# Kernel optimization log

Hardware: AMD Instinct MI355X
Metric: run time of the kernel (lower is better)

## Reference

```python
import jax, jax.numpy as jnp
import numpy as np

N = 4096      # total instances in the bag
S = 64        # number of images (segments), idx_list has S+1 boundaries
L = 500
D = 128
FLAT = 50 * 4 * 4  # 800


def _conv(x, w, b):
    # x: [N,C,H,W], w: [O,I,5,5], VALID conv, stride 1
    y = jax.lax.conv_general_dilated(x, w, (1, 1), 'VALID',
                                     dimension_numbers=('NCHW', 'OIHW', 'NCHW'))
    return y + b[None, :, None, None]


def _maxpool2(x):
    return jax.lax.reduce_window(x, -jnp.inf, jax.lax.max,
                                 (1, 1, 2, 2), (1, 1, 2, 2), 'VALID')


def setup_inputs() -> dict:
    key = jax.random.key(0)
    ks = jax.random.split(key, 18)
    def p(k, shape, fan):
        return jax.random.normal(k, shape, jnp.float32) * np.float32(1.0 / np.sqrt(fan))
    x = jax.random.normal(ks[0], (1, N, 3, 28, 28), jnp.float32)
    idx_list = (jnp.arange(S + 1, dtype=jnp.int32) * (N // S))  # sorted boundaries 0..N
    return {
        'x': x,
        'idx_list': idx_list,
        'conv1_w': p(ks[1], (20, 3, 5, 5), 3 * 25), 'conv1_b': jnp.zeros((20,), jnp.float32),
        'conv2_w': p(ks[2], (50, 20, 5, 5), 20 * 25), 'conv2_b': jnp.zeros((50,), jnp.float32),
        'fc_w': p(ks[3], (FLAT, L), FLAT), 'fc_b': jnp.zeros((L,), jnp.float32),
        'a1_w1': p(ks[4], (L, D), L), 'a1_b1': jnp.zeros((D,), jnp.float32),
        'a1_w2': p(ks[5], (D, 1), D), 'a1_b2': jnp.zeros((1,), jnp.float32),
        'a2_w1': p(ks[6], (L, D), L), 'a2_b1': jnp.zeros((D,), jnp.float32),
        'a2_w2': p(ks[7], (D, 1), D), 'a2_b2': jnp.zeros((1,), jnp.float32),
        'clf_w': p(ks[8], (L, 1), L), 'clf_b': jnp.zeros((1,), jnp.float32),
    }


def reference(x, idx_list, conv1_w, conv1_b, conv2_w, conv2_b, fc_w, fc_b,
              a1_w1, a1_b1, a1_w2, a1_b2, a2_w1, a2_b1, a2_w2, a2_b2,
              clf_w, clf_b):
    xs = x[0]                                         # squeeze(0): [N,3,28,28]
    h = _maxpool2(jax.nn.relu(_conv(xs, conv1_w, conv1_b)))   # [N,20,12,12]
    h = _maxpool2(jax.nn.relu(_conv(h, conv2_w, conv2_b)))    # [N,50,4,4]
    H = jax.nn.relu(h.reshape(-1, FLAT) @ fc_w + fc_b)        # [N,L]

    def attn1(z):
        return jnp.tanh(z @ a1_w1 + a1_b1) @ a1_w2 + a1_b2    # [.,1]

    A = attn1(H).T                                    # [1,N] (returned raw, pre-softmax)

    # ragged per-segment softmax pooling (replaces the Python loop)
    n = H.shape[0]
    seg = jnp.searchsorted(idx_list[1:], jnp.arange(n, dtype=idx_list.dtype), side='right')
    a = attn1(H)[:, 0]                                # [N] scores (same math as per-segment recompute)
    seg_max = jax.ops.segment_max(a, seg, num_segments=S)
    e = jnp.exp(a - seg_max[seg])
    denom = jax.ops.segment_sum(e, seg, num_segments=S)
    w = e / denom[seg]                                # per-segment softmax weights
    instance_f = jax.ops.segment_sum(w[:, None] * H, seg, num_segments=S)  # [S,L]

    b_att = jnp.tanh(instance_f @ a2_w1 + a2_b1) @ a2_w2 + a2_b2  # [S,1]
    B = jax.nn.softmax(b_att[:, 0])[None, :]          # [1,S]
    bag_feature = B @ instance_f                      # [1,L]
    Y_prob = jax.nn.sigmoid(bag_feature @ clf_w + clf_b)  # [1,1]
    Y_hat = (Y_prob >= 0.5).astype(jnp.float32)
    return (Y_prob, Y_hat, A)
```

## Files before the change

### kernel.cpp

```cpp
#include <hip/hip_runtime.h>
#include <math.h>

typedef _Float16 f16x8 __attribute__((ext_vector_type(8)));
typedef float    f32x4 __attribute__((ext_vector_type(4)));

static __device__ __forceinline__ unsigned short f2h(float f) {
  _Float16 h = (_Float16)f;
  return __builtin_bit_cast(unsigned short, h);
}

__global__ __launch_bounds__(256) void k_prep_all(const float* __restrict__ c1w,
                                                  const float* __restrict__ c2w,
                                                  const float* __restrict__ fcw,
                                                  const float* __restrict__ a1w1,
                                                  unsigned short* __restrict__ Wc1g,
                                                  unsigned short* __restrict__ Wg,
                                                  unsigned short* __restrict__ Wtfc,
                                                  unsigned short* __restrict__ Wt1) {
  int i = blockIdx.x * 256 + threadIdx.x;
  if (i < 6400) {
    int kh = i / 1280, r = i % 1280;
    int co = r / 40, q = r % 40;
    int kw = q >> 2, ci = q & 3;
    Wc1g[i] = f2h((co < 20 && ci < 3 && kw < 5) ? c1w[((co * 3 + ci) * 5 + kh) * 5 + kw] : 0.f);
    return;
  }
  i -= 6400;
  if (i < 38400) {
    int tap = i / 1536, r = i % 1536;
    int co = r / 24, ci = r % 24;
    Wg[i] = f2h((co < 50 && ci < 20) ? c2w[(co * 20 + ci) * 25 + tap] : 0.f);
    return;
  }
  i -= 38400;
  if (i < 409600) {
    int kt = i >> 14, r = i & 16383;
    int nn = r >> 5, kk = r & 31;
    int k = kt * 32 + kk;
    Wtfc[i] = f2h((nn < 500) ? fcw[k * 500 + nn] : 0.f);
    return;
  }
  i -= 409600;
  if (i < 65536) {
    int kt = i >> 12, r = i & 4095;
    int col = r >> 5, kk = r & 31;
    int k = kt * 32 + kk;
    Wt1[i] = f2h((k < 500) ? a1w1[k * 128 + col] : 0.f);
  }
}

__global__ __launch_bounds__(64, 2) void k_conv12(const float* __restrict__ x,
                                                  const unsigned short* __restrict__ Wc1g,
                                                  const float* __restrict__ cb1,
                                                  const unsigned short* __restrict__ Wg,
                                                  const float* __restrict__ cb2,
                                                  unsigned short* __restrict__ flat16) {
  __shared__ unsigned short xcl[3200];
  __shared__ unsigned short h1s[3472];
  int tid = threadIdx.x;
  int n = blockIdx.x;
  int r16 = tid & 15, g = tid >> 4;

  if (tid < 16) h1s[3456 + tid] = 0;
  xcl[3136 + tid] = 0;
  {
    const float* xg = x + (size_t)n * 2352;
    for (int p = tid; p < 784; p += 64) {
      unsigned int lo = (unsigned int)f2h(xg[p]) | ((unsigned int)f2h(xg[784 + p]) << 16);
      unsigned int hi = (unsigned int)f2h(xg[1568 + p]);
      uint2 v; v.x = lo; v.y = hi;
      *(uint2*)(xcl + 4 * p) = v;
    }
  }
  __syncthreads();

  {
    f16x8 bv[5][2];
    #pragma unroll
    for (int kh = 0; kh < 5; kh++) {
      bv[kh][0] = __builtin_bit_cast(f16x8, *(const uint4*)(Wc1g + (kh * 32 + r16) * 40 + 8 * g));
      bv[kh][1] = __builtin_bit_cast(f16x8, *(const uint4*)(Wc1g + (kh * 32 + 16 + r16) * 40 + 8 * g));
    }
    float bias0 = cb1[r16];
    float bias1 = (r16 < 4) ? cb1[16 + r16] : 0.f;
    int ay = (r16 >> 3), ax = (r16 & 7) + 2 * g;

    for (int chunk = 0; chunk < 9; ++chunk) {
      f32x4 acc[4][2];
      #pragma unroll
      for (int ti = 0; ti < 4; ti++) {
        acc[ti][0] = (f32x4){0.f, 0.f, 0.f, 0.f};
        acc[ti][1] = (f32x4){0.f, 0.f, 0.f, 0.f};
      }
      #pragma unroll
      for (int kh = 0; kh < 5; kh++) {
        #pragma unroll
        for (int ti = 0; ti < 4; ti++) {
          int t = chunk * 4 + ti;
          int ty = t / 3, tx = t - ty * 3;
          int oy = 2 * ty + ay + kh;
          int ox = 8 * tx + ax;
          const unsigned short* p = xcl + (oy * 28 + ox) * 4;
          uint2 lo = *(const uint2*)p;
          uint2 hi = *(const uint2*)(p + 4);
          uint4 af; af.x = lo.x; af.y = lo.y; af.z = hi.x; af.w = hi.y;
          f16x8 av = __builtin_bit_cast(f16x8, af);
          acc[ti][0] = __builtin_amdgcn_mfma_f32_16x16x32_f16(av, bv[kh][0], acc[ti][0], 0, 0, 0);
          acc[ti][1] = __builtin_amdgcn_mfma_f32_16x16x32_f16(av, bv[kh][1], acc[ti][1], 0, 0, 0);
        }
      }
      #pragma unroll
      for (int ti = 0; ti < 4; ti++) {
        int t = chunk * 4 + ti;
        int ty = t / 3, tx = t - ty * 3;
        #pragma unroll
        for (int nt = 0; nt < 2; nt++) {
          int co = 16 * nt + r16;
          f32x4 c = acc[ti][nt];
          float h0 = fmaxf(c[0], c[1]);
          float h1 = fmaxf(c[2], c[3]);
          float v0 = fmaxf(h0, __shfl_xor(h0, 32));
          float v1 = fmaxf(h1, __shfl_xor(h1, 32));
          if (g < 2 && co < 24) {
            float bias = nt ? bias1 : bias0;
            v0 = fmaxf(v0 + bias, 0.f);
            v1 = fmaxf(v1 + bias, 0.f);
            int px0 = 4 * tx + 2 * g;
            unsigned short* o = h1s + (ty * 12 + px0) * 24 + co;
            o[0]  = f2h(v0);
            o[24] = f2h(v1);
          }
        }
      }
    }
  }
  __syncthreads();

  {
    float cbias0 = cb2[r16];
    float cbias1 = cb2[16 + r16];
    float cbias2 = cb2[32 + r16];
    float cbias3 = (r16 < 2) ? cb2[48 + r16] : 0.f;

    f32x4 acc[4][4];
    #pragma unroll
    for (int mt = 0; mt < 4; mt++)
      #pragma unroll
      for (int nt = 0; nt < 4; nt++) acc[mt][nt] = (f32x4){0.f, 0.f, 0.f, 0.f};

    uint4 FAa[4], FAb[4], FBa[4], FBb[4];
    auto load_frags = [&](uint4* A, uint4* B, int tap) {
      int kh = tap / 5, kw = tap % 5;
      #pragma unroll
      for (int nt = 0; nt < 4; nt++) {
        uint4 u = make_uint4(0, 0, 0, 0);
        if (g < 3) {
          int co = 16 * nt + r16;
          u = *(const uint4*)(Wg + tap * 1536 + co * 24 + 8 * g);
        }
        B[nt] = u;
      }
      #pragma unroll
      for (int mt = 0; mt < 4; mt++) {
        int posl = mt * 16 + r16;
        int oy = posl >> 3, ox = posl & 7;
        A[mt] = *(const uint4*)(h1s + ((oy + kh) * 12 + (ox + kw)) * 24 + 8 * g);
      }
    };
    auto mma = [&](const uint4* A, const uint4* B) {
      #pragma unroll
      for (int mt = 0; mt < 4; mt++) {
        f16x8 av = __builtin_bit_cast(f16x8, A[mt]);
        #pragma unroll
        for (int nt = 0; nt < 4; nt++) {
          acc[mt][nt] = __builtin_amdgcn_mfma_f32_16x16x32_f16(
              av, __builtin_bit_cast(f16x8, B[nt]), acc[mt][nt], 0, 0, 0);
        }
      }
    };

    load_frags(FAa, FAb, 0);
    for (int tap = 0; tap < 25; tap += 2) {
      if (tap + 1 < 25) load_frags(FBa, FBb, tap + 1);
      mma(FAa, FAb);
      if (tap + 2 < 25) load_frags(FAa, FAb, tap + 2);
      if (tap + 1 < 25) mma(FBa, FBb);
    }

    #pragma unroll
    for (int mt = 0; mt < 4; mt++) {
      #pragma unroll
      for (int nt = 0; nt < 4; nt++) {
        int co = 16 * nt + r16;
        f32x4 c = acc[mt][nt];
        float h0 = fmaxf(c[0], c[1]);
        float h1 = fmaxf(c[2], c[3]);
        float v0 = fmaxf(h0, __shfl_xor(h0, 32));
        float v1 = fmaxf(h1, __shfl_xor(h1, 32));
        if (g < 2 && co < 50) {
          float bias = (nt == 0) ? cbias0 : (nt == 1) ? cbias1 : (nt == 2) ? cbias2 : cbias3;
          v0 = fmaxf(v0 + bias, 0.f);
          v1 = fmaxf(v1 + bias, 0.f);
          unsigned short* o = flat16 + ((size_t)n * 50 + co) * 16 + mt * 4 + 2 * g;
          o[0] = f2h(v0);
          o[1] = f2h(v1);
        }
      }
    }
  }
}

__global__ __launch_bounds__(256) void k_fc_mfma(const unsigned short* __restrict__ flat16,
                                                 const unsigned short* __restrict__ Wt,
                                                 const float* __restrict__ b,
                                                 float* __restrict__ H,
                                                 unsigned short* __restrict__ H16) {
  int tid = threadIdx.x;
  int wave = tid >> 6, lane = tid & 63;
  int r16 = lane & 15, g = lane >> 4;
  int bm = blockIdx.x & 15, bn = blockIdx.x >> 4;
  int m0 = bm * 256 + wave * 64;
  int n0 = bn * 32;

  f32x4 acc[4][2];
  #pragma unroll
  for (int mt = 0; mt < 4; mt++) {
    acc[mt][0] = (f32x4){0.f, 0.f, 0.f, 0.f};
    acc[mt][1] = (f32x4){0.f, 0.f, 0.f, 0.f};
  }

  const unsigned short* Abase = flat16 + (size_t)(m0 + r16) * 800 + 8 * g;
  const unsigned short* Bbase = Wt + (size_t)(n0 + r16) * 32 + 8 * g;

  for (int kt = 0; kt < 25; kt++) {
    uint4 bf0 = *(const uint4*)(Bbase + kt * 16384);
    uint4 bf1 = *(const uint4*)(Bbase + kt * 16384 + 512);
    f16x8 bv0 = __builtin_bit_cast(f16x8, bf0);
    f16x8 bv1 = __builtin_bit_cast(f16x8, bf1);
    #pragma unroll
    for (int mt = 0; mt < 4; mt++) {
      uint4 af = *(const uint4*)(Abase + mt * 12800 + kt * 32);
      f16x8 av = __builtin_bit_cast(f16x8, af);
      acc[mt][0] = __builtin_amdgcn_mfma_f32_16x16x32_f16(av, bv0, acc[mt][0], 0, 0, 0);
      acc[mt][1] = __builtin_amdgcn_mfma_f32_16x16x32_f16(av, bv1, acc[mt][1], 0, 0, 0);
    }
  }

  #pragma unroll
  for (int nt = 0; nt < 2; nt++) {
    int col = n0 + nt * 16 + r16;
    bool real = col < 500;
    float bias = real ? b[col] : 0.f;
    #pragma unroll
    for (int mt = 0; mt < 4; mt++) {
      #pragma unroll
      for (int j = 0; j < 4; j++) {
        int row = m0 + mt * 16 + 4 * g + j;
        float val = fmaxf(acc[mt][nt][j] + bias, 0.f);
        if (real) H[(size_t)row * 500 + col] = val;
        H16[(size_t)row * 512 + col] = f2h(val);
      }
    }
  }
}

__global__ __launch_bounds__(64) void k_attn1_mfma(const unsigned short* __restrict__ H16,
                                                   const unsigned short* __restrict__ Wt1,
                                                   const float* __restrict__ b1,
                                                   const float* __restrict__ w2,
                                                   const float* __restrict__ b2,
                                                   float* __restrict__ a,
                                                   float* __restrict__ outA) {
  int lane = threadIdx.x;
  int r16 = lane & 15, g = lane >> 4;
  int m0 = blockIdx.x * 32;

  f32x4 acc[2][8];
  #pragma unroll
  for (int mt = 0; mt < 2; mt++)
    #pragma unroll
    for (int nt = 0; nt < 8; nt++) acc[mt][nt] = (f32x4){0.f, 0.f, 0.f, 0.f};

  const unsigned short* Abase = H16 + (size_t)(m0 + r16) * 512 + 8 * g;
  const unsigned short* Bbase = Wt1 + r16 * 32 + 8 * g;

  for (int kt = 0; kt < 16; kt++) {
    uint4 a0 = *(const uint4*)(Abase + kt * 32);
    uint4 a1 = *(const uint4*)(Abase + 16 * 512 + kt * 32);
    f16x8 av0 = __builtin_bit_cast(f16x8, a0);
    f16x8 av1 = __builtin_bit_cast(f16x8, a1);
    #pragma unroll
    for (int nt = 0; nt < 8; nt++) {
      uint4 bf = *(const uint4*)(Bbase + kt * 4096 + nt * 512);
      f16x8 bv = __builtin_bit_cast(f16x8, bf);
      acc[0][nt] = __builtin_amdgcn_mfma_f32_16x16x32_f16(av0, bv, acc[0][nt], 0, 0, 0);
      acc[1][nt] = __builtin_amdgcn_mfma_f32_16x16x32_f16(av1, bv, acc[1][nt], 0, 0, 0);
    }
  }

  float b1v[8], w2v[8];
  #pragma unroll
  for (int nt = 0; nt < 8; nt++) {
    int col = nt * 16 + r16;
    b1v[nt] = b1[col];
    w2v[nt] = w2[col];
  }
  float bb2 = b2[0];

  #pragma unroll
  for (int mt = 0; mt < 2; mt++) {
    float part[4];
    #pragma unroll
    for (int j = 0; j < 4; j++) {
      float s = 0.f;
      #pragma unroll
      for (int nt = 0; nt < 8; nt++)
        s += tanhf(acc[mt][nt][j] + b1v[nt]) * w2v[nt];
      part[j] = s;
    }
    #pragma unroll
    for (int off = 1; off < 16; off <<= 1) {
      #pragma unroll
      for (int j = 0; j < 4; j++) part[j] += __shfl_xor(part[j], off);
    }
    if (r16 == 0) {
      #pragma unroll
      for (int j = 0; j < 4; j++) {
        int row = m0 + mt * 16 + 4 * g + j;
        float val = part[j] + bb2;
        a[row] = val;
        outA[row] = val;
      }
    }
  }
}

__global__ __launch_bounds__(256) void k_segpool(const float* __restrict__ a,
                                                 const float* __restrict__ H,
                                                 const int* __restrict__ idx,
                                                 float* __restrict__ instf) {
  __shared__ float red[4];
  __shared__ float sval;
  int s = blockIdx.x, tid = threadIdx.x;
  int i0 = idx[s], i1 = idx[s + 1];
  float mx = -INFINITY;
  for (int i = i0 + tid; i < i1; i += 256) mx = fmaxf(mx, a[i]);
  #pragma unroll
  for (int off = 32; off > 0; off >>= 1) mx = fmaxf(mx, __shfl_down(mx, off));
  if ((tid & 63) == 0) red[tid >> 6] = mx;
  __syncthreads();
  if (tid == 0) sval = fmaxf(fmaxf(red[0], red[1]), fmaxf(red[2], red[3]));
  __syncthreads();
  float m = sval;
  float sm = 0.f;
  for (int i = i0 + tid; i < i1; i += 256) sm += expf(a[i] - m);
  #pragma unroll
  for (int off = 32; off > 0; off >>= 1) sm += __shfl_down(sm, off);
  if ((tid & 63) == 0) red[tid >> 6] = sm;
  __syncthreads();
  if (tid == 0) sval = red[0] + red[1] + red[2] + red[3];
  __syncthreads();
  float inv = 1.f / sval;
  if (tid < 250) {
    float acc0 = 0.f, acc1 = 0.f;
    for (int i = i0; i < i1; i++) {
      float e = expf(a[i] - m) * inv;
      acc0 += e * H[(size_t)i * 500 + tid];
      acc1 += e * H[(size_t)i * 500 + tid + 250];
    }
    instf[s * 500 + tid] = acc0;
    instf[s * 500 + tid + 250] = acc1;
  }
}

__global__ __launch_bounds__(512) void k_batt(const float* __restrict__ instf,
                                              const float* __restrict__ w1,
                                              const float* __restrict__ b1,
                                              const float* __restrict__ w2,
                                              const float* __restrict__ b2,
                                              float* __restrict__ batt) {
  __shared__ float fs[500];
  __shared__ float part[512];
  __shared__ float red[2];
  int s = blockIdx.x, tid = threadIdx.x;
  for (int i = tid; i < 500; i += 512) fs[i] = instf[s * 500 + i];
  __syncthreads();
  int c = tid & 127, q = tid >> 7;
  float t = 0.f;
  int k0 = q * 125;
  #pragma unroll 5
  for (int k = k0; k < k0 + 125; k++) t += fs[k] * w1[k * 128 + c];
  part[tid] = t;
  __syncthreads();
  if (tid < 128) {
    float tt = part[tid] + part[tid + 128] + part[tid + 256] + part[tid + 384] + b1[tid];
    float v = tanhf(tt) * w2[tid];
    #pragma unroll
    for (int off = 32; off > 0; off >>= 1) v += __shfl_down(v, off);
    if ((tid & 63) == 0) red[tid >> 6] = v;
  }
  __syncthreads();
  if (tid == 0) batt[s] = red[0] + red[1] + b2[0];
}

__global__ __launch_bounds__(256) void k_final(const float* __restrict__ batt,
                                               const float* __restrict__ instf,
                                               const float* __restrict__ clfw,
                                               const float* __restrict__ clfb,
                                               float* __restrict__ out) {
  __shared__ float Bsh[64];
  __shared__ float red[4];
  int tid = threadIdx.x;
  if (tid < 64) {
    float v = batt[tid];
    float mx = v;
    #pragma unroll
    for (int off = 32; off > 0; off >>= 1) mx = fmaxf(mx, __shfl_xor(mx, off));
    float e = expf(v - mx);
    float smv = e;
    #pragma unroll
    for (int off = 32; off > 0; off >>= 1) smv += __shfl_xor(smv, off);
    Bsh[tid] = e / smv;
  }
  __syncthreads();
  float part = 0.f;
  if (tid < 250) {
    float bag0 = 0.f, bag1 = 0.f;
    #pragma unroll 4
    for (int s2 = 0; s2 < 64; s2++) {
      float Bv = Bsh[s2];
      bag0 += Bv * instf[s2 * 500 + tid];
      bag1 += Bv * instf[s2 * 500 + tid + 250];
    }
    part = bag0 * clfw[tid] + bag1 * clfw[tid + 250];
  }
  #pragma unroll
  for (int off = 32; off > 0; off >>= 1) part += __shfl_down(part, off);
  if ((tid & 63) == 0) red[tid >> 6] = part;
  __syncthreads();
  if (tid == 0) {
    float z = red[0] + red[1] + red[2] + red[3] + clfb[0];
    out[0] = 1.f / (1.f + expf(-z));
    out[1] = (z >= 0.f) ? 1.f : 0.f;
  }
}

extern "C" void kernel_launch(void* const* d_in, const int* in_sizes, int n_in,
                              void* d_out, int out_size, void* d_ws, size_t ws_size,
                              hipStream_t stream) {
  const float* x       = (const float*)d_in[0];
  const int*   idx     = (const int*)d_in[1];
  const float* conv1_w = (const float*)d_in[2];
  const float* conv1_b = (const float*)d_in[3];
  const float* conv2_w = (const float*)d_in[4];
  const float* conv2_b = (const float*)d_in[5];
  const float* fc_w    = (const float*)d_in[6];
  const float* fc_b    = (const float*)d_in[7];
  const float* a1_w1   = (const float*)d_in[8];
  const float* a1_b1   = (const float*)d_in[9];
  const float* a1_w2   = (const float*)d_in[10];
  const float* a1_b2   = (const float*)d_in[11];
  const float* a2_w1   = (const float*)d_in[12];
  const float* a2_b1   = (const float*)d_in[13];
  const float* a2_w2   = (const float*)d_in[14];
  const float* a2_b2   = (const float*)d_in[15];
  const float* clf_w   = (const float*)d_in[16];
  const float* clf_b   = (const float*)d_in[17];
  float* out = (float*)d_out;

  int N = in_sizes[0] / 2352;
  int S = in_sizes[1] - 1;

  float* wsf   = (float*)d_ws;
  float* H     = wsf;
  float* a     = H + (size_t)N * 500;
  float* instf = a + N;
  float* batt  = instf + (size_t)S * 500;
  unsigned short* Wg    = (unsigned short*)(batt + S + 8);
  unsigned short* Wc1g  = Wg + 38400;
  unsigned short* Wtfc  = Wc1g + 6400;
  unsigned short* Wt1   = Wtfc + 409600;
  unsigned short* flat16= Wt1 + 65536;
  unsigned short* H16   = flat16 + (size_t)N * 800;

  k_prep_all<<<2031, 256, 0, stream>>>(conv1_w, conv2_w, fc_w, a1_w1, Wc1g, Wg, Wtfc, Wt1);
  k_conv12<<<N, 64, 0, stream>>>(x, Wc1g, conv1_b, Wg, conv2_b, flat16);
  k_fc_mfma<<<256, 256, 0, stream>>>(flat16, Wtfc, fc_b, H, H16);
  k_attn1_mfma<<<N / 32, 64, 0, stream>>>(H16, Wt1, a1_b1, a1_w2, a1_b2, a, out + 2);
  k_segpool<<<S, 256, 0, stream>>>(a, H, idx, instf);
  k_batt<<<S, 512, 0, stream>>>(instf, a2_w1, a2_b1, a2_w2, a2_b2, batt);
  k_final<<<1, 256, 0, stream>>>(batt, instf, clf_w, clf_b, out);
}
```

Before: 153.8 us.

## Split conv blocks across two waves and fuse segment pooling with bag attention

The conv kernel now runs two waves per image: conv1 chunks are interleaved between the waves and conv2 output rows are split so each wave computes half the M tiles. The input load is batched into registers before conversion to fp16. The segment-pool and bag-attention kernels are merged into one 512-thread kernel that keeps instance features in shared memory, saving a launch and a global round trip. The conv change raises per-block parallelism and cuts per-wave serial work, at the cost of more threads per block.

After: 149.7 us. 2.6% less time.

```diff
diff --git a/kernel.cpp b/kernel.cpp
--- a/kernel.cpp
+++ b/kernel.cpp
@@ -49,27 +49,38 @@
   }
 }
 
-__global__ __launch_bounds__(64, 2) void k_conv12(const float* __restrict__ x,
-                                                  const unsigned short* __restrict__ Wc1g,
-                                                  const float* __restrict__ cb1,
-                                                  const unsigned short* __restrict__ Wg,
-                                                  const float* __restrict__ cb2,
-                                                  unsigned short* __restrict__ flat16) {
+__global__ __launch_bounds__(128, 2) void k_conv12(const float* __restrict__ x,
+                                                   const unsigned short* __restrict__ Wc1g,
+                                                   const float* __restrict__ cb1,
+                                                   const unsigned short* __restrict__ Wg,
+                                                   const float* __restrict__ cb2,
+                                                   unsigned short* __restrict__ flat16) {
   __shared__ unsigned short xcl[3200];
   __shared__ unsigned short h1s[3472];
   int tid = threadIdx.x;
   int n = blockIdx.x;
-  int r16 = tid & 15, g = tid >> 4;
+  int w = tid >> 6;
+  int lane = tid & 63;
+  int r16 = lane & 15, g = lane >> 4;
 
   if (tid < 16) h1s[3456 + tid] = 0;
-  xcl[3136 + tid] = 0;
+  if (tid < 64) xcl[3136 + tid] = 0;
   {
     const float* xg = x + (size_t)n * 2352;
-    for (int p = tid; p < 784; p += 64) {
-      unsigned int lo = (unsigned int)f2h(xg[p]) | ((unsigned int)f2h(xg[784 + p]) << 16);
-      unsigned int hi = (unsigned int)f2h(xg[1568 + p]);
-      uint2 v; v.x = lo; v.y = hi;
-      *(uint2*)(xcl + 4 * p) = v;
+    float v0[7], v1[7], v2[7];
+    #pragma unroll
+    for (int i = 0; i < 7; ++i) {
+      int p = tid + i * 128;
+      if (p < 784) { v0[i] = xg[p]; v1[i] = xg[784 + p]; v2[i] = xg[1568 + p]; }
+    }
+    #pragma unroll
+    for (int i = 0; i < 7; ++i) {
+      int p = tid + i * 128;
+      if (p < 784) {
+        unsigned int lo = (unsigned int)f2h(v0[i]) | ((unsigned int)f2h(v1[i]) << 16);
+        uint2 vv; vv.x = lo; vv.y = (unsigned int)f2h(v2[i]);
+        *(uint2*)(xcl + 4 * p) = vv;
+      }
     }
   }
   __syncthreads();
@@ -85,7 +96,7 @@
     float bias1 = (r16 < 4) ? cb1[16 + r16] : 0.f;
     int ay = (r16 >> 3), ax = (r16 & 7) + 2 * g;
 
-    for (int chunk = 0; chunk < 9; ++chunk) {
+    for (int chunk = w; chunk < 9; chunk += 2) {
       f32x4 acc[4][2];
       #pragma unroll
       for (int ti = 0; ti < 4; ti++) {
@@ -142,13 +153,13 @@
     float cbias2 = cb2[32 + r16];
     float cbias3 = (r16 < 2) ? cb2[48 + r16] : 0.f;
 
-    f32x4 acc[4][4];
-    #pragma unroll
-    for (int mt = 0; mt < 4; mt++)
+    f32x4 acc[2][4];
+    #pragma unroll
+    for (int mt = 0; mt < 2; mt++)
       #pragma unroll
       for (int nt = 0; nt < 4; nt++) acc[mt][nt] = (f32x4){0.f, 0.f, 0.f, 0.f};
 
-    uint4 FAa[4], FAb[4], FBa[4], FBb[4];
+    uint4 FAa[2], FAb[4], FBa[2], FBb[4];
     auto load_frags = [&](uint4* A, uint4* B, int tap) {
       int kh = tap / 5, kw = tap % 5;
       #pragma unroll
@@ -161,15 +172,15 @@
         B[nt] = u;
       }
       #pragma unroll
-      for (int mt = 0; mt < 4; mt++) {
-        int posl = mt * 16 + r16;
+      for (int mtp = 0; mtp < 2; mtp++) {
+        int posl = (2 * w + mtp) * 16 + r16;
         int oy = posl >> 3, ox = posl & 7;
-        A[mt] = *(const uint4*)(h1s + ((oy + kh) * 12 + (ox + kw)) * 24 + 8 * g);
+        A[mtp] = *(const uint4*)(h1s + ((oy + kh) * 12 + (ox + kw)) * 24 + 8 * g);
       }
     };
     auto mma = [&](const uint4* A, const uint4* B) {
       #pragma unroll
-      for (int mt = 0; mt < 4; mt++) {
+      for (int mt = 0; mt < 2; mt++) {
         f16x8 av = __builtin_bit_cast(f16x8, A[mt]);
         #pragma unroll
         for (int nt = 0; nt < 4; nt++) {
@@ -188,11 +199,12 @@
     }
 
     #pragma unroll
-    for (int mt = 0; mt < 4; mt++) {
+    for (int mtp = 0; mtp < 2; mtp++) {
+      int py = 2 * w + mtp;
       #pragma unroll
       for (int nt = 0; nt < 4; nt++) {
         int co = 16 * nt + r16;
-        f32x4 c = acc[mt][nt];
+        f32x4 c = acc[mtp][nt];
         float h0 = fmaxf(c[0], c[1]);
         float h1 = fmaxf(c[2], c[3]);
         float v0 = fmaxf(h0, __shfl_xor(h0, 32));
@@ -201,7 +213,7 @@
           float bias = (nt == 0) ? cbias0 : (nt == 1) ? cbias1 : (nt == 2) ? cbias2 : cbias3;
           v0 = fmaxf(v0 + bias, 0.f);
           v1 = fmaxf(v1 + bias, 0.f);
-          unsigned short* o = flat16 + ((size_t)n * 50 + co) * 16 + mt * 4 + 2 * g;
+          unsigned short* o = flat16 + ((size_t)n * 50 + co) * 16 + py * 4 + 2 * g;
           o[0] = f2h(v0);
           o[1] = f2h(v1);
         }
@@ -335,30 +347,48 @@
   }
 }
 
-__global__ __launch_bounds__(256) void k_segpool(const float* __restrict__ a,
+__global__ __launch_bounds__(512) void k_segbatt(const float* __restrict__ a,
                                                  const float* __restrict__ H,
                                                  const int* __restrict__ idx,
-                                                 float* __restrict__ instf) {
-  __shared__ float red[4];
+                                                 const float* __restrict__ w1,
+                                                 const float* __restrict__ b1,
+                                                 const float* __restrict__ w2,
+                                                 const float* __restrict__ b2,
+                                                 float* __restrict__ instf,
+                                                 float* __restrict__ batt) {
+  __shared__ float fs[500];
+  __shared__ float part[512];
+  __shared__ float red[8];
   __shared__ float sval;
   int s = blockIdx.x, tid = threadIdx.x;
   int i0 = idx[s], i1 = idx[s + 1];
+
   float mx = -INFINITY;
-  for (int i = i0 + tid; i < i1; i += 256) mx = fmaxf(mx, a[i]);
+  for (int i = i0 + tid; i < i1; i += 512) mx = fmaxf(mx, a[i]);
   #pragma unroll
   for (int off = 32; off > 0; off >>= 1) mx = fmaxf(mx, __shfl_down(mx, off));
   if ((tid & 63) == 0) red[tid >> 6] = mx;
   __syncthreads();
-  if (tid == 0) sval = fmaxf(fmaxf(red[0], red[1]), fmaxf(red[2], red[3]));
+  if (tid == 0) {
+    float m2 = red[0];
+    #pragma unroll
+    for (int j = 1; j < 8; j++) m2 = fmaxf(m2, red[j]);
+    sval = m2;
+  }
   __syncthreads();
   float m = sval;
   float sm = 0.f;
-  for (int i = i0 + tid; i < i1; i += 256) sm += expf(a[i] - m);
+  for (int i = i0 + tid; i < i1; i += 512) sm += expf(a[i] - m);
   #pragma unroll
   for (int off = 32; off > 0; off >>= 1) sm += __shfl_down(sm, off);
   if ((tid & 63) == 0) red[tid >> 6] = sm;
   __syncthreads();
-  if (tid == 0) sval = red[0] + red[1] + red[2] + red[3];
+  if (tid == 0) {
+    float t2 = 0.f;
+    #pragma unroll
+    for (int j = 0; j < 8; j++) t2 += red[j];
+    sval = t2;
+  }
   __syncthreads();
   float inv = 1.f / sval;
   if (tid < 250) {
@@ -370,20 +400,9 @@
     }
     instf[s * 500 + tid] = acc0;
     instf[s * 500 + tid + 250] = acc1;
-  }
-}
-
-__global__ __launch_bounds__(512) void k_batt(const float* __restrict__ instf,
-                                              const float* __restrict__ w1,
-                                              const float* __restrict__ b1,
-                                              const float* __restrict__ w2,
-                                              const float* __restrict__ b2,
-                                              float* __restrict__ batt) {
-  __shared__ float fs[500];
-  __shared__ float part[512];
-  __shared__ float red[2];
-  int s = blockIdx.x, tid = threadIdx.x;
-  for (int i = tid; i < 500; i += 512) fs[i] = instf[s * 500 + i];
+    fs[tid] = acc0;
+    fs[tid + 250] = acc1;
+  }
   __syncthreads();
   int c = tid & 127, q = tid >> 7;
   float t = 0.f;
@@ -484,10 +503,9 @@
   unsigned short* H16   = flat16 + (size_t)N * 800;
 
   k_prep_all<<<2031, 256, 0, stream>>>(conv1_w, conv2_w, fc_w, a1_w1, Wc1g, Wg, Wtfc, Wt1);
-  k_conv12<<<N, 64, 0, stream>>>(x, Wc1g, conv1_b, Wg, conv2_b, flat16);
+  k_conv12<<<N, 128, 0, stream>>>(x, Wc1g, conv1_b, Wg, conv2_b, flat16);
   k_fc_mfma<<<256, 256, 0, stream>>>(flat16, Wtfc, fc_b, H, H16);
   k_attn1_mfma<<<N / 32, 64, 0, stream>>>(H16, Wt1, a1_b1, a1_w2, a1_b2, a, out + 2);
-  k_segpool<<<S, 256, 0, stream>>>(a, H, idx, instf);
-  k_batt<<<S, 512, 0, stream>>>(instf, a2_w1, a2_b1, a2_w2, a2_b2, batt);
+  k_segbatt<<<S, 512, 0, stream>>>(a, H, idx, a2_w1, a2_b1, a2_w2, a2_b2, instf, batt);
   k_final<<<1, 256, 0, stream>>>(batt, instf, clf_w, clf_b, out);
 }
```
